# Optimization experiments

Hardware: AMD Instinct MI355X
Metric: run time of the kernel (lower is better)

## Reference

```python
import jax, jax.numpy as jnp
import numpy as np

HIDDEN = 768
NUM_HEADS = 12
HEAD_DIM = HIDDEN // NUM_HEADS  # 64
BATCH = 1
SEQ = 4096


def setup_inputs() -> dict:
    key = jax.random.key(0)
    ks = jax.random.split(key, 10)
    s = 0.02
    return {
        "hidden_states": jax.random.normal(ks[0], (BATCH, SEQ, HIDDEN), dtype=jnp.float32),
        "attention_mask": jnp.zeros((BATCH, 1, 1, SEQ), dtype=jnp.float32),
        "q_w": jax.random.normal(ks[1], (HIDDEN, HIDDEN), dtype=jnp.float32) * s,
        "q_b": jnp.zeros((HIDDEN,), dtype=jnp.float32),
        "k_w": jax.random.normal(ks[2], (HIDDEN, HIDDEN), dtype=jnp.float32) * s,
        "k_b": jnp.zeros((HIDDEN,), dtype=jnp.float32),
        "v_w": jax.random.normal(ks[3], (HIDDEN, HIDDEN), dtype=jnp.float32) * s,
        "v_b": jnp.zeros((HIDDEN,), dtype=jnp.float32),
        "out_w": jax.random.normal(ks[4], (HIDDEN, HIDDEN), dtype=jnp.float32) * s,
        "out_b": jnp.zeros((HIDDEN,), dtype=jnp.float32),
    }


def reference(hidden_states, attention_mask, q_w, q_b, k_w, k_b, v_w, v_b, out_w, out_b):
    B, S, _ = hidden_states.shape
    scale = 1.0 / np.sqrt(HEAD_DIM).astype(np.float32)

    def split_heads(x):
        # [B, S, H*D] -> [B, H, S, D]
        return x.reshape(B, S, NUM_HEADS, HEAD_DIM).transpose(0, 2, 1, 3)

    q = split_heads(hidden_states @ q_w.T + q_b)
    k = split_heads(hidden_states @ k_w.T + k_b)
    v = split_heads(hidden_states @ v_w.T + v_b)

    # [B, H, S, S] score tensor (materialized, as in the original module)
    scores = jnp.einsum("bhqd,bhkd->bhqk", q, k) * scale + attention_mask
    probs = jax.nn.softmax(scores, axis=-1)
    ctx = jnp.einsum("bhqk,bhkd->bhqd", probs, v)
    ctx = ctx.transpose(0, 2, 1, 3).reshape(B, S, HIDDEN)
    return ctx @ out_w.T + out_b
```

## Files before the change

### kernel.cpp

```cpp
#include <hip/hip_runtime.h>
#include <hip/hip_bf16.h>

#define SEQ  4096
#define HID  768
#define NH   12
#define HD   64
#define QKVN 2304
#define KVB  32
#define SPLIT 4
#define NT   ((SEQ/SPLIT)/KVB)
#define LOG2E 1.44269504f

typedef __attribute__((ext_vector_type(8)))  short  short8;
typedef __attribute__((ext_vector_type(4)))  float  f32x4;
typedef __attribute__((ext_vector_type(16))) float  f32x16;

static __device__ __forceinline__ unsigned short bf16b(float x) {
  __hip_bfloat16 h = __float2bfloat16(x);
  return *reinterpret_cast<unsigned short*>(&h);
}
static __device__ __forceinline__ unsigned pkbf(float lo, float hi) {
  return (unsigned)bf16b(lo) | ((unsigned)bf16b(hi) << 16);
}
static __device__ __forceinline__ void store4(__hip_bfloat16* p, float a, float b, float c, float d) {
  unsigned long long v = (unsigned long long)pkbf(a, b) | ((unsigned long long)pkbf(c, d) << 32);
  *reinterpret_cast<unsigned long long*>(p) = v;
}
static __device__ __forceinline__ void gload16(const void* g, void* l) {
  __builtin_amdgcn_global_load_lds(
      (const __attribute__((address_space(1))) void*)g,
      (__attribute__((address_space(3))) void*)l, 16, 0, 0);
}

#if __has_builtin(__builtin_amdgcn_exp2f)
#define EXP2(x) __builtin_amdgcn_exp2f(x)
#else
#define EXP2(x) __expf((x) * 0.6931472f)
#endif

static __device__ __forceinline__ void swap32(unsigned a, unsigned b, unsigned& x, unsigned& y) {
#if __has_builtin(__builtin_amdgcn_permlane32_swap)
  auto r = __builtin_amdgcn_permlane32_swap((int)a, (int)b, false, false);
  x = (unsigned)r[0]; y = (unsigned)r[1];
#else
  unsigned pa = (unsigned)__shfl_xor((int)a, 32);
  unsigned pb = (unsigned)__shfl_xor((int)b, 32);
  int hi = (int)((threadIdx.x & 63) >> 5);
  x = hi ? pb : a;
  y = hi ? b : pa;
#endif
}

static __device__ __forceinline__ void cvt_store(float* p, float v) { *p = v; }
static __device__ __forceinline__ void cvt_store(__hip_bfloat16* p, float v) { *p = __float2bfloat16(v); }

__global__ __launch_bounds__(256) void prep_kernel(
    const float* __restrict__ hs,
    const float* __restrict__ qw, const float* __restrict__ kw,
    const float* __restrict__ vw, const float* __restrict__ ow,
    const float* __restrict__ qb, const float* __restrict__ kb,
    const float* __restrict__ vb, const float* __restrict__ msk,
    __hip_bfloat16* __restrict__ Xb,
    __hip_bfloat16* __restrict__ Wqkv,
    __hip_bfloat16* __restrict__ Wo,
    float* __restrict__ bqkv,
    float* __restrict__ mask2)
{
  const int NX = SEQ*HID/4, NW = QKVN*HID/4, NO = HID*HID/4, NB = QKVN/4, NM = SEQ/4;
  int idx = blockIdx.x*256 + threadIdx.x;
  if (idx < NX) {
    float4 v = ((const float4*)hs)[idx];
    store4(Xb + idx*4, v.x, v.y, v.z, v.w);
  } else if (idx < NX + NW) {
    int f = (idx - NX)*4;
    int row = f / HID, col = f - row*HID;
    const float* src = (row < HID)   ? qw + row*HID + col
                     : (row < 2*HID) ? kw + (row-HID)*HID + col
                     :                 vw + (row-2*HID)*HID + col;
    float4 v = *(const float4*)src;
    store4(Wqkv + f, v.x, v.y, v.z, v.w);
  } else if (idx < NX + NW + NO) {
    int li = idx - NX - NW;
    float4 v = ((const float4*)ow)[li];
    store4(Wo + li*4, v.x, v.y, v.z, v.w);
  } else if (idx < NX + NW + NO + NB) {
    int f = (idx - NX - NW - NO)*4;
    const float* src = (f < HID) ? qb + f : (f < 2*HID) ? kb + (f-HID) : vb + (f-2*HID);
    *(float4*)(bqkv + f) = *(const float4*)src;
  } else if (idx < NX + NW + NO + NB + NM) {
    int f = (idx - NX - NW - NO - NB)*4;
    float4 v = *(const float4*)(msk + f);
    float4 o; o.x = v.x*LOG2E; o.y = v.y*LOG2E; o.z = v.z*LOG2E; o.w = v.w*LOG2E;
    *(float4*)(mask2 + f) = o;
  }
}

template <typename OutT>
__global__ __launch_bounds__(256) void gemm_nt(
    const __hip_bfloat16* __restrict__ A,
    const __hip_bfloat16* __restrict__ B,
    const float* __restrict__ bias,
    OutT* __restrict__ C, int N, int K)
{
  __shared__ __align__(16) short As[128*32];
  __shared__ __align__(16) short Bs[128*32];
  const int tid  = threadIdx.x;
  const int lane = tid & 63;
  const int w    = tid >> 6;
  const int m0   = blockIdx.y * 128;
  const int n0   = blockIdx.x * 128;
  const int wrow = w >> 1, wcol = w & 1;
  const int l15  = lane & 15;
  const int k8   = (lane >> 4) * 8;

  f32x4 acc[4][4] = {};

  const int base0 = w*512;
  const int base1 = (4+w)*512;
  const int f0 = base0 + lane*8, f1 = base1 + lane*8;
  const __hip_bfloat16* Ap0 = A + (long)(m0 + (f0>>5))*K + (f0&31);
  const __hip_bfloat16* Ap1 = A + (long)(m0 + (f1>>5))*K + (f1&31);
  const __hip_bfloat16* Bp0 = B + (long)(n0 + (f0>>5))*K + (f0&31);
  const __hip_bfloat16* Bp1 = B + (long)(n0 + (f1>>5))*K + (f1&31);

  for (int k0 = 0; k0 < K; k0 += 32) {
    gload16(Ap0 + k0, As + base0);
    gload16(Ap1 + k0, As + base1);
    gload16(Bp0 + k0, Bs + base0);
    gload16(Bp1 + k0, Bs + base1);
    __syncthreads();

    short8 af[4], bfm[4];
#pragma unroll
    for (int mi = 0; mi < 4; ++mi)
      af[mi] = *(const short8*)&As[(wrow*64 + mi*16 + l15)*32 + k8];
#pragma unroll
    for (int ni = 0; ni < 4; ++ni)
      bfm[ni] = *(const short8*)&Bs[(wcol*64 + ni*16 + l15)*32 + k8];
#pragma unroll
    for (int mi = 0; mi < 4; ++mi)
#pragma unroll
      for (int ni = 0; ni < 4; ++ni)
        acc[mi][ni] = __builtin_amdgcn_mfma_f32_16x16x32_bf16(af[mi], bfm[ni], acc[mi][ni], 0, 0, 0);
    __syncthreads();
  }

  const int rbase = (lane >> 4) * 4;
#pragma unroll
  for (int mi = 0; mi < 4; ++mi)
#pragma unroll
    for (int ni = 0; ni < 4; ++ni) {
      int gm = m0 + wrow*64 + mi*16 + rbase;
      int gn = n0 + wcol*64 + ni*16 + l15;
      float bv = bias[gn];
#pragma unroll
      for (int r = 0; r < 4; ++r)
        cvt_store(&C[(long)(gm + r)*N + gn], acc[mi][ni][r] + bv);
    }
}

__global__ __launch_bounds__(128, 4) void attn_fwd(
    const __hip_bfloat16* __restrict__ QKV,
    const float* __restrict__ mask2,
    float* __restrict__ Oacc,
    float* __restrict__ Lacc)
{
  __shared__ __align__(16) char SMEM[18432];
  short* KsB = (short*)SMEM;
  short* VTB = (short*)(SMEM + 8192);
  float* Of  = (float*)SMEM;

  const int tid  = threadIdx.x;
  const int lane = tid & 63;
  const int wv   = tid >> 6;
  const int head = blockIdx.y;
  const int qt   = blockIdx.x;
  const int s0   = blockIdx.z * (SEQ/SPLIT);
  const int q0   = qt*64 + wv*32;
  const int ql   = lane & 31;
  const int hi   = lane >> 5;
  const float scale2 = 0.125f * LOG2E;

  short8 qf[4];
  {
    const __hip_bfloat16* qrow = QKV + (long)(q0+ql)*QKVN + head*HD + hi*8;
#pragma unroll
    for (int dc = 0; dc < 4; ++dc)
      qf[dc] = *(const short8*)(qrow + dc*16);
  }

  const __hip_bfloat16* kp[2];
#pragma unroll
  for (int i = 0; i < 2; ++i) {
    int slot = i*128 + tid;
    int krow = slot >> 3, kcs = slot & 7;
    kp[i] = QKV + (long)(s0 + krow)*QKVN + HID + head*HD + ((kcs ^ (krow & 7))*8);
  }

  const int vkv2 = (tid & 15)*2, vdb = (tid >> 4)*8;
  const __hip_bfloat16* vsrc = QKV + (long)(s0 + vkv2)*QKVN + 2*HID + head*HD + vdb;

  f32x16 oacc[2] = {};
  float lrun = 0.0f;
  float4 mgc[4], mgn[4];

  short8 va = *(const short8*)(vsrc);
  short8 vb = *(const short8*)(vsrc + QKVN);
#pragma unroll
  for (int e = 0; e < 8; ++e) {
    unsigned w0 = (unsigned)(unsigned short)va[e] | ((unsigned)(unsigned short)vb[e] << 16);
    *(unsigned*)&VTB[(vdb + e)*40 + vkv2] = w0;
  }
  gload16(kp[0], KsB + (0*128 + wv*64)*8);
  gload16(kp[1], KsB + (1*128 + wv*64)*8);
  __builtin_amdgcn_sched_barrier(0);
  {
    const __hip_bfloat16* pv = vsrc + (long)KVB*QKVN;
    va = *(const short8*)(pv);
    vb = *(const short8*)(pv + QKVN);
#pragma unroll
    for (int g = 0; g < 4; ++g)
      mgc[g] = *(const float4*)(mask2 + s0 + 8*g + 4*hi);
  }
  asm volatile("s_waitcnt vmcnt(6) lgkmcnt(0)" ::: "memory");
  __builtin_amdgcn_s_barrier();
  __builtin_amdgcn_sched_barrier(0);

  for (int t = 0; t < NT; ++t) {
    const int cur = t & 1, nxt = cur ^ 1;
    short* ksC = KsB + cur*2048;
    short* vtC = VTB + cur*2560;

    short* vtN = VTB + nxt*2560;
#pragma unroll
    for (int e = 0; e < 8; ++e) {
      unsigned w0 = (unsigned)(unsigned short)va[e] | ((unsigned)(unsigned short)vb[e] << 16);
      *(unsigned*)&vtN[(vdb + e)*40 + vkv2] = w0;
    }
    if (t + 1 < NT) {
      const long kn = (long)(t+1) * KVB * QKVN;
      short* ksN = KsB + nxt*2048;
      gload16(kp[0] + kn, ksN + (0*128 + wv*64)*8);
      gload16(kp[1] + kn, ksN + (1*128 + wv*64)*8);
    }
    __builtin_amdgcn_sched_barrier(0);
    {
      const long kn2 = (long)(((t+2) < NT) ? (t+2) : (NT-1)) * KVB * QKVN;
      va = *(const short8*)(vsrc + kn2);
      vb = *(const short8*)(vsrc + kn2 + QKVN);
      const float* mrowN = mask2 + s0 + (((t+1) < NT) ? (t+1) : t)*KVB;
#pragma unroll
      for (int g = 0; g < 4; ++g)
        mgn[g] = *(const float4*)(mrowN + 8*g + 4*hi);
    }

    short8 kf[4];
#pragma unroll
    for (int dc = 0; dc < 4; ++dc)
      kf[dc] = *(const short8*)&ksC[ql*64 + (((dc*2 + hi) ^ (ql & 7))*8)];
    f32x16 sacc = {};
#pragma unroll
    for (int dc = 0; dc < 4; ++dc)
      sacc = __builtin_amdgcn_mfma_f32_32x32x16_bf16(kf[dc], qf[dc], sacc, 0, 0, 0);

    float p[16];
#pragma unroll
    for (int g = 0; g < 4; ++g) {
      p[4*g+0] = EXP2(sacc[4*g+0]*scale2 + mgc[g].x);
      p[4*g+1] = EXP2(sacc[4*g+1]*scale2 + mgc[g].y);
      p[4*g+2] = EXP2(sacc[4*g+2]*scale2 + mgc[g].z);
      p[4*g+3] = EXP2(sacc[4*g+3]*scale2 + mgc[g].w);
    }
    float sl0 = 0.f, sl1 = 0.f;
#pragma unroll
    for (int r = 0; r < 8; ++r) { sl0 += p[r]; sl1 += p[8+r]; }
    lrun += sl0 + sl1;

    unsigned pk[8];
#pragma unroll
    for (int u = 0; u < 8; ++u) pk[u] = pkbf(p[2*u], p[2*u+1]);
    unsigned b0[4], b1[4];
    swap32(pk[0], pk[2], b0[0], b0[2]);
    swap32(pk[1], pk[3], b0[1], b0[3]);
    swap32(pk[4], pk[6], b1[0], b1[2]);
    swap32(pk[5], pk[7], b1[1], b1[3]);
    union U { unsigned u[4]; short8 s; };
    U pb0{{b0[0], b0[1], b0[2], b0[3]}};
    U pb1{{b1[0], b1[1], b1[2], b1[3]}};

    short8 a00 = *(const short8*)&vtC[(ql)*40      + hi*8];
    short8 a01 = *(const short8*)&vtC[(ql)*40 + 16 + hi*8];
    short8 a10 = *(const short8*)&vtC[(32+ql)*40      + hi*8];
    short8 a11 = *(const short8*)&vtC[(32+ql)*40 + 16 + hi*8];

    oacc[0] = __builtin_amdgcn_mfma_f32_32x32x16_bf16(a00, pb0.s, oacc[0], 0, 0, 0);
    oacc[0] = __builtin_amdgcn_mfma_f32_32x32x16_bf16(a01, pb1.s, oacc[0], 0, 0, 0);
    oacc[1] = __builtin_amdgcn_mfma_f32_32x32x16_bf16(a10, pb0.s, oacc[1], 0, 0, 0);
    oacc[1] = __builtin_amdgcn_mfma_f32_32x32x16_bf16(a11, pb1.s, oacc[1], 0, 0, 0);

#pragma unroll
    for (int g = 0; g < 4; ++g) mgc[g] = mgn[g];

    asm volatile("s_waitcnt vmcnt(6) lgkmcnt(0)" ::: "memory");
    __builtin_amdgcn_s_barrier();
    __builtin_amdgcn_sched_barrier(0);
  }

  float lp = lrun + __shfl_xor(lrun, 32);
  if (hi == 0)
    unsafeAtomicAdd(&Lacc[head*SEQ + q0 + ql], lp);

#pragma unroll
  for (int cb = 0; cb < 2; ++cb)
#pragma unroll
    for (int g = 0; g < 4; ++g)
#pragma unroll
      for (int r = 0; r < 4; ++r)
        Of[(wv*32 + ql)*65 + cb*32 + 8*g + 4*hi + r] = oacc[cb][4*g + r];
  __syncthreads();

  const int qbase = qt*64;
  float* orow = Oacc + (long)qbase*HID + head*HD + lane;
#pragma unroll 4
  for (int r = 0; r < 32; ++r) {
    int q = wv*32 + r;
    unsafeAtomicAdd(orow + (long)q*HID, Of[q*65 + lane]);
  }
}

__global__ __launch_bounds__(256) void finalize_kernel(
    const float* __restrict__ Oacc, const float* __restrict__ Lacc,
    __hip_bfloat16* __restrict__ ctx)
{
  int idx = blockIdx.x*256 + threadIdx.x;
  int q  = idx / (HID/4);
  int c4 = (idx - q*(HID/4))*4;
  float inv = 1.0f / Lacc[(c4 >> 6)*SEQ + q];
  float4 o = *(const float4*)&Oacc[(long)q*HID + c4];
  store4(ctx + (long)q*HID + c4, o.x*inv, o.y*inv, o.z*inv, o.w*inv);
}

extern "C" void kernel_launch(void* const* d_in, const int* in_sizes, int n_in,
                              void* d_out, int out_size, void* d_ws, size_t ws_size,
                              hipStream_t stream) {
  const float* hs  = (const float*)d_in[0];
  const float* msk = (const float*)d_in[1];
  const float* qw  = (const float*)d_in[2];
  const float* qb  = (const float*)d_in[3];
  const float* kw  = (const float*)d_in[4];
  const float* kb  = (const float*)d_in[5];
  const float* vw  = (const float*)d_in[6];
  const float* vb  = (const float*)d_in[7];
  const float* ow  = (const float*)d_in[8];
  const float* ob  = (const float*)d_in[9];

  char* ws = (char*)d_ws;
  __hip_bfloat16* Xb   = (__hip_bfloat16*)(ws);
  __hip_bfloat16* Wqkv = (__hip_bfloat16*)(ws + 6291456);
  __hip_bfloat16* Wo   = (__hip_bfloat16*)(ws + 9830400);
  float*          bqkv = (float*)         (ws + 11010048);
  __hip_bfloat16* QKV  = (__hip_bfloat16*)(ws + 11019264);
  __hip_bfloat16* Ctx  = (__hip_bfloat16*)(ws + 29893632);
  float*          Oacc = (float*)         (ws + 36185088);
  float*          Lacc = (float*)         (ws + 48768000);
  float*          Mask2= (float*)         (ws + 48964608);

  hipMemsetAsync(Oacc, 0, 12582912 + 196608, stream);

  {
    const int total = SEQ*HID/4 + QKVN*HID/4 + HID*HID/4 + QKVN/4 + SEQ/4;
    prep_kernel<<<(total + 255)/256, 256, 0, stream>>>(hs, qw, kw, vw, ow, qb, kb, vb, msk,
                                                       Xb, Wqkv, Wo, bqkv, Mask2);
  }
  gemm_nt<__hip_bfloat16><<<dim3(QKVN/128, SEQ/128), 256, 0, stream>>>(Xb, Wqkv, bqkv, QKV, QKVN, HID);
  attn_fwd<<<dim3(SEQ/64, NH, SPLIT), 128, 0, stream>>>(QKV, Mask2, Oacc, Lacc);
  finalize_kernel<<<(SEQ*HID/4)/256, 256, 0, stream>>>(Oacc, Lacc, Ctx);
  gemm_nt<float><<<dim3(HID/128, SEQ/128), 256, 0, stream>>>(Ctx, Wo, ob, (float*)d_out, HID, HID);
}
```

Baseline: 179.7 us.

## Single-buffer V^T tile and shrink attention LDS footprint with setprio around MFMAs

The attention kernel stops double-buffering the transposed V tile in LDS. It now writes the next V tile after a barrier at the end of each iteration and adds a second barrier before compute, while K stays double-buffered. The output staging epilogue runs in two phases of 32 rows so the reduced 13 KB LDS allocation suffices. This is meant to allow more resident blocks per CU. MFMA sections are wrapped in s_setprio, and the cost is an extra barrier per KV tile plus less overlap of the V transpose with compute.

```diff
diff --git a/kernel.cpp b/kernel.cpp
--- a/kernel.cpp
+++ b/kernel.cpp
@@ -165,7 +165,7 @@
     float* __restrict__ Oacc,
     float* __restrict__ Lacc)
 {
-  __shared__ __align__(16) char SMEM[18432];
+  __shared__ __align__(16) char SMEM[13312];
   short* KsB = (short*)SMEM;
   short* VTB = (short*)(SMEM + 8192);
   float* Of  = (float*)SMEM;
@@ -215,53 +215,30 @@
   gload16(kp[1], KsB + (1*128 + wv*64)*8);
   __builtin_amdgcn_sched_barrier(0);
   {
+#pragma unroll
+    for (int g = 0; g < 4; ++g)
+      mgc[g] = *(const float4*)(mask2 + s0 + 8*g + 4*hi);
     const __hip_bfloat16* pv = vsrc + (long)KVB*QKVN;
     va = *(const short8*)(pv);
     vb = *(const short8*)(pv + QKVN);
-#pragma unroll
-    for (int g = 0; g < 4; ++g)
-      mgc[g] = *(const float4*)(mask2 + s0 + 8*g + 4*hi);
   }
   asm volatile("s_waitcnt vmcnt(6) lgkmcnt(0)" ::: "memory");
   __builtin_amdgcn_s_barrier();
   __builtin_amdgcn_sched_barrier(0);
 
   for (int t = 0; t < NT; ++t) {
-    const int cur = t & 1, nxt = cur ^ 1;
-    short* ksC = KsB + cur*2048;
-    short* vtC = VTB + cur*2560;
-
-    short* vtN = VTB + nxt*2560;
-#pragma unroll
-    for (int e = 0; e < 8; ++e) {
-      unsigned w0 = (unsigned)(unsigned short)va[e] | ((unsigned)(unsigned short)vb[e] << 16);
-      *(unsigned*)&vtN[(vdb + e)*40 + vkv2] = w0;
-    }
-    if (t + 1 < NT) {
-      const long kn = (long)(t+1) * KVB * QKVN;
-      short* ksN = KsB + nxt*2048;
-      gload16(kp[0] + kn, ksN + (0*128 + wv*64)*8);
-      gload16(kp[1] + kn, ksN + (1*128 + wv*64)*8);
-    }
-    __builtin_amdgcn_sched_barrier(0);
-    {
-      const long kn2 = (long)(((t+2) < NT) ? (t+2) : (NT-1)) * KVB * QKVN;
-      va = *(const short8*)(vsrc + kn2);
-      vb = *(const short8*)(vsrc + kn2 + QKVN);
-      const float* mrowN = mask2 + s0 + (((t+1) < NT) ? (t+1) : t)*KVB;
-#pragma unroll
-      for (int g = 0; g < 4; ++g)
-        mgn[g] = *(const float4*)(mrowN + 8*g + 4*hi);
-    }
+    short* ksC = KsB + (t & 1)*2048;
 
     short8 kf[4];
 #pragma unroll
     for (int dc = 0; dc < 4; ++dc)
       kf[dc] = *(const short8*)&ksC[ql*64 + (((dc*2 + hi) ^ (ql & 7))*8)];
     f32x16 sacc = {};
+    __builtin_amdgcn_s_setprio(1);
 #pragma unroll
     for (int dc = 0; dc < 4; ++dc)
       sacc = __builtin_amdgcn_mfma_f32_32x32x16_bf16(kf[dc], qf[dc], sacc, 0, 0, 0);
+    __builtin_amdgcn_s_setprio(0);
 
     float p[16];
 #pragma unroll
@@ -288,22 +265,46 @@
     U pb0{{b0[0], b0[1], b0[2], b0[3]}};
     U pb1{{b1[0], b1[1], b1[2], b1[3]}};
 
-    short8 a00 = *(const short8*)&vtC[(ql)*40      + hi*8];
-    short8 a01 = *(const short8*)&vtC[(ql)*40 + 16 + hi*8];
-    short8 a10 = *(const short8*)&vtC[(32+ql)*40      + hi*8];
-    short8 a11 = *(const short8*)&vtC[(32+ql)*40 + 16 + hi*8];
-
+    short8 a00 = *(const short8*)&VTB[(ql)*40      + hi*8];
+    short8 a01 = *(const short8*)&VTB[(ql)*40 + 16 + hi*8];
+    short8 a10 = *(const short8*)&VTB[(32+ql)*40      + hi*8];
+    short8 a11 = *(const short8*)&VTB[(32+ql)*40 + 16 + hi*8];
+
+    __builtin_amdgcn_s_setprio(1);
     oacc[0] = __builtin_amdgcn_mfma_f32_32x32x16_bf16(a00, pb0.s, oacc[0], 0, 0, 0);
     oacc[0] = __builtin_amdgcn_mfma_f32_32x32x16_bf16(a01, pb1.s, oacc[0], 0, 0, 0);
     oacc[1] = __builtin_amdgcn_mfma_f32_32x32x16_bf16(a10, pb0.s, oacc[1], 0, 0, 0);
     oacc[1] = __builtin_amdgcn_mfma_f32_32x32x16_bf16(a11, pb1.s, oacc[1], 0, 0, 0);
-
-#pragma unroll
-    for (int g = 0; g < 4; ++g) mgc[g] = mgn[g];
-
-    asm volatile("s_waitcnt vmcnt(6) lgkmcnt(0)" ::: "memory");
+    __builtin_amdgcn_s_setprio(0);
+
+    asm volatile("s_waitcnt lgkmcnt(0)" ::: "memory");
     __builtin_amdgcn_s_barrier();
     __builtin_amdgcn_sched_barrier(0);
+
+    if (t + 1 < NT) {
+#pragma unroll
+      for (int e = 0; e < 8; ++e) {
+        unsigned w0 = (unsigned)(unsigned short)va[e] | ((unsigned)(unsigned short)vb[e] << 16);
+        *(unsigned*)&VTB[(vdb + e)*40 + vkv2] = w0;
+      }
+      const long kn = (long)(t+1) * KVB * QKVN;
+      short* ksN = KsB + ((t+1) & 1)*2048;
+      gload16(kp[0] + kn, ksN + (0*128 + wv*64)*8);
+      gload16(kp[1] + kn, ksN + (1*128 + wv*64)*8);
+      __builtin_amdgcn_sched_barrier(0);
+      const float* mrowN = mask2 + s0 + (t+1)*KVB;
+#pragma unroll
+      for (int g = 0; g < 4; ++g)
+        mgn[g] = *(const float4*)(mrowN + 8*g + 4*hi);
+      const long kn2 = (long)(((t+2) < NT) ? (t+2) : (NT-1)) * KVB * QKVN;
+      va = *(const short8*)(vsrc + kn2);
+      vb = *(const short8*)(vsrc + kn2 + QKVN);
+#pragma unroll
+      for (int g = 0; g < 4; ++g) mgc[g] = mgn[g];
+      asm volatile("s_waitcnt vmcnt(6) lgkmcnt(0)" ::: "memory");
+      __builtin_amdgcn_s_barrier();
+      __builtin_amdgcn_sched_barrier(0);
+    }
   }
 
   float lp = lrun + __shfl_xor(lrun, 32);
@@ -311,20 +312,24 @@
     unsafeAtomicAdd(&Lacc[head*SEQ + q0 + ql], lp);
 
 #pragma unroll
-  for (int cb = 0; cb < 2; ++cb)
-#pragma unroll
-    for (int g = 0; g < 4; ++g)
-#pragma unroll
-      for (int r = 0; r < 4; ++r)
-        Of[(wv*32 + ql)*65 + cb*32 + 8*g + 4*hi + r] = oacc[cb][4*g + r];
-  __syncthreads();
-
-  const int qbase = qt*64;
-  float* orow = Oacc + (long)qbase*HID + head*HD + lane;
+  for (int ph = 0; ph < 2; ++ph) {
+    __syncthreads();
+    if (wv == ph) {
+#pragma unroll
+      for (int cb = 0; cb < 2; ++cb)
+#pragma unroll
+        for (int g = 0; g < 4; ++g)
+#pragma unroll
+          for (int r = 0; r < 4; ++r)
+            Of[ql*65 + cb*32 + 8*g + 4*hi + r] = oacc[cb][4*g + r];
+    }
+    __syncthreads();
+    float* obase = Oacc + (long)(qt*64 + ph*32)*HID + head*HD + lane;
 #pragma unroll 4
-  for (int r = 0; r < 32; ++r) {
-    int q = wv*32 + r;
-    unsafeAtomicAdd(orow + (long)q*HID, Of[q*65 + lane]);
+    for (int r = 0; r < 16; ++r) {
+      int row = wv*16 + r;
+      unsafeAtomicAdd(obase + (long)row*HID, Of[row*65 + lane]);
+    }
   }
 }
 
```

Result: slower. 186.3 us (+3.7%).
